# Optimization experiments

Hardware: AMD Instinct MI355X
Metric: run time of the kernel (lower is better)

The kernel has to match this reference:

```python
import jax, jax.numpy as jnp
import numpy as np

B, N, C_IN, S = 8, 50000, 32, 9
C_OUT, M, NNZ = 64, 12500, 50000


def setup_inputs() -> dict:
    key = jax.random.key(0)
    ks = jax.random.split(key, 6)
    return {
        "x": jax.random.normal(ks[0], (B, N, C_IN), dtype=jnp.float32),
        "W": jax.random.normal(ks[1], (S * C_IN, C_OUT), dtype=jnp.float32) * 0.05,
        "b": jnp.zeros((C_OUT,), dtype=jnp.float32),
        "value": jax.random.uniform(ks[2], (NNZ,), dtype=jnp.float32),
        "spiral_indices": jax.random.randint(ks[3], (N, S), 0, N),
        "row": jax.random.randint(ks[4], (NNZ,), 0, M),
        "col": jax.random.randint(ks[5], (NNZ,), 0, N),
        "dim_size": M,
    }


def reference(x, W, b, value, spiral_indices, row, col, dim_size):
    Bb, Nn, Ci = x.shape
    # SpiralConv: gather spiral neighborhoods then linear
    g = x[:, spiral_indices]                # [B, N, S, C_in]
    h = g.reshape(Bb, Nn, -1) @ W + b       # [B, N, C_out]
    h = jax.nn.elu(h)                       # ELU, alpha=1
    # Pool: sparse down-transform (index_select * value, scatter_add over rows)
    gathered = h[:, col] * value[None, :, None]            # [B, nnz, C_out]
    pooled = jax.ops.segment_sum(
        gathered.transpose(1, 0, 2), row, num_segments=dim_size
    ).transpose(1, 0, 2)                                   # [B, M, C_out]
    return pooled
```

## Files before the change

### kernel.cpp

```cpp
#include <hip/hip_runtime.h>
#include <hip/hip_bf16.h>
#include <math.h>

#define Bq    8
#define Nq    50000
#define CIN   32
#define Sq    9
#define COUT  64
#define MSEG  12500
#define NNZq  50000
#define KSTEPS 9

#define WT_BYTES  65536
#define XB_BYTES  ((size_t)Bq*Nq*CIN*2)

typedef __bf16 bf16x8 __attribute__((ext_vector_type(8)));
typedef float  f32x4  __attribute__((ext_vector_type(4)));

static __device__ __forceinline__ unsigned short f2bf(float f) {
  union { float f; unsigned u; } v; v.f = f;
  unsigned r = v.u + 0x7fffu + ((v.u >> 16) & 1u);
  return (unsigned short)(r >> 16);
}

__global__ __launch_bounds__(256) void prep_wt(const float* __restrict__ W,
                                               unsigned short* __restrict__ WT)
{
  int t = blockIdx.x * 256 + threadIdx.x;
  if (t >= 288 * 64) return;
  int c = t & 63;
  int k = t >> 6;
  int j = (c & 3) * 16 + (c >> 2);
  WT[j * 288 + k] = f2bf(W[k * 64 + c]);
}

__global__ __launch_bounds__(256) void prep_xb(const float* __restrict__ x,
                                               unsigned short* __restrict__ xb)
{
  int i = blockIdx.x * 256 + threadIdx.x;
  float4 v = ((const float4*)x)[i];
  ushort4 p;
  p.x = f2bf(v.x); p.y = f2bf(v.y); p.z = f2bf(v.z); p.w = f2bf(v.w);
  ((ushort4*)xb)[i] = p;
}

__global__ __launch_bounds__(256) void csr_hist(const int* __restrict__ row,
                                                int* __restrict__ cnt)
{
  int e = blockIdx.x * 256 + threadIdx.x;
  if (e < NNZq) atomicAdd(&cnt[row[e]], 1);
}

__global__ __launch_bounds__(1024) void csr_scan(const int* __restrict__ cnt,
                                                 int* __restrict__ start)
{
  __shared__ int s[1024];
  const int t = threadIdx.x;
  const int PER = (MSEG + 1023) / 1024;
  int loc[PER];
  int sum = 0;
  #pragma unroll
  for (int i = 0; i < PER; ++i) {
    int r = t * PER + i;
    int v = (r < MSEG) ? cnt[r] : 0;
    loc[i] = sum; sum += v;
  }
  s[t] = sum; __syncthreads();
  for (int off = 1; off < 1024; off <<= 1) {
    int v = (t >= off) ? s[t - off] : 0;
    __syncthreads();
    s[t] += v;
    __syncthreads();
  }
  int pre = (t == 0) ? 0 : s[t - 1];
  #pragma unroll
  for (int i = 0; i < PER; ++i) {
    int r = t * PER + i;
    if (r < MSEG) start[r] = pre + loc[i];
  }
}

__global__ __launch_bounds__(256) void csr_fill(const int* __restrict__ row,
                                                const int* __restrict__ start,
                                                int* __restrict__ fill,
                                                int* __restrict__ eidx)
{
  int e = blockIdx.x * 256 + threadIdx.x;
  if (e >= NNZq) return;
  int r = row[e];
  int p = start[r] + atomicAdd(&fill[r], 1);
  eidx[p] = e;
}

__global__ __launch_bounds__(256, 4) void fused_gather_gemm_elu(
    const unsigned short* __restrict__ xb, const unsigned short* __restrict__ WT,
    const float* __restrict__ bias, const int* __restrict__ sidx,
    unsigned short* __restrict__ h, int bbase, int nb, int lgnb)
{
  const int tid  = threadIdx.x;
  const int bid  = blockIdx.x;
  const int bloc = bid & (nb - 1);
  const int n0   = (bid >> lgnb) * 64;
  const int b    = bbase + bloc;

  const int w  = tid >> 6;
  const int l  = tid & 63;
  const int la = l & 15;
  const int kg = l >> 4;

  int nrow   = n0 + w * 16 + la;
  int nclamp = nrow < Nq ? nrow : Nq - 1;

  int idxs[KSTEPS];
  #pragma unroll
  for (int s = 0; s < KSTEPS; ++s) idxs[s] = sidx[nclamp * Sq + s];

  const unsigned short* xbb = xb + (size_t)b * Nq * CIN + kg * 8;
  const __bf16* wb = (const __bf16*)WT + la * 288 + kg * 8;

  bf16x8 afr[KSTEPS];
  #pragma unroll
  for (int ks = 0; ks < KSTEPS; ++ks)
    afr[ks] = *(const bf16x8*)(xbb + (size_t)idxs[ks] * CIN);

  f32x4 acc[4];
  #pragma unroll
  for (int i = 0; i < 4; ++i) acc[i] = (f32x4){0.f, 0.f, 0.f, 0.f};

  #pragma unroll
  for (int ks = 0; ks < KSTEPS; ++ks) {
    #pragma unroll
    for (int ct = 0; ct < 4; ++ct) {
      bf16x8 bb = *(const bf16x8*)(wb + ct * 16 * 288 + ks * 32);
      acc[ct] = __builtin_amdgcn_mfma_f32_16x16x32_bf16(afr[ks], bb, acc[ct], 0, 0, 0);
    }
  }

  float4 b4 = ((const float4*)bias)[la];
  #pragma unroll
  for (int r = 0; r < 4; ++r) {
    int n = n0 + w * 16 + kg * 4 + r;
    if (n < Nq) {
      float v0 = acc[0][r] + b4.x;
      float v1 = acc[1][r] + b4.y;
      float v2 = acc[2][r] + b4.z;
      float v3 = acc[3][r] + b4.w;
      v0 = v0 > 0.f ? v0 : (__expf(v0) - 1.0f);
      v1 = v1 > 0.f ? v1 : (__expf(v1) - 1.0f);
      v2 = v2 > 0.f ? v2 : (__expf(v2) - 1.0f);
      v3 = v3 > 0.f ? v3 : (__expf(v3) - 1.0f);
      ushort4 pk;
      pk.x = f2bf(v0); pk.y = f2bf(v1); pk.z = f2bf(v2); pk.w = f2bf(v3);
      *(ushort4*)&h[((size_t)n * nb + bloc) * COUT + 4 * la] = pk;
    }
  }
}

__global__ __launch_bounds__(512) void csr_pool(
    const unsigned short* __restrict__ h, const float* __restrict__ value,
    const int* __restrict__ col, const int* __restrict__ start,
    const int* __restrict__ cnt, const int* __restrict__ eidx,
    float* __restrict__ out, int bbase, int nb)
{
  int r    = blockIdx.x;
  int c    = threadIdx.x & 63;
  int bloc = threadIdx.x >> 6;
  int s0 = start[r];
  int ne = cnt[r];
  float acc = 0.f;
  int j = 0;
  for (; j + 4 <= ne; j += 4) {
    int e0 = eidx[s0+j], e1 = eidx[s0+j+1], e2 = eidx[s0+j+2], e3 = eidx[s0+j+3];
    int   c0 = col[e0],   c1 = col[e1],   c2 = col[e2],   c3 = col[e3];
    float v0 = value[e0], v1 = value[e1], v2 = value[e2], v3 = value[e3];
    unsigned short h0 = h[((size_t)c0 * nb + bloc) * COUT + c];
    unsigned short h1 = h[((size_t)c1 * nb + bloc) * COUT + c];
    unsigned short h2 = h[((size_t)c2 * nb + bloc) * COUT + c];
    unsigned short h3 = h[((size_t)c3 * nb + bloc) * COUT + c];
    acc += v0 * __bfloat162float(*(const __hip_bfloat16*)&h0)
         + v1 * __bfloat162float(*(const __hip_bfloat16*)&h1)
         + v2 * __bfloat162float(*(const __hip_bfloat16*)&h2)
         + v3 * __bfloat162float(*(const __hip_bfloat16*)&h3);
  }
  for (; j < ne; ++j) {
    int e = eidx[s0 + j];
    float v = value[e];
    int cc = col[e];
    unsigned short hv = h[((size_t)cc * nb + bloc) * COUT + c];
    acc += v * __bfloat162float(*(const __hip_bfloat16*)&hv);
  }
  out[((size_t)(bbase + bloc) * MSEG + r) * COUT + c] = acc;
}

extern "C" void kernel_launch(void* const* d_in, const int* in_sizes, int n_in,
                              void* d_out, int out_size, void* d_ws, size_t ws_size,
                              hipStream_t stream)
{
  const float* x     = (const float*)d_in[0];
  const float* W     = (const float*)d_in[1];
  const float* bias  = (const float*)d_in[2];
  const float* value = (const float*)d_in[3];
  const int*   sidx  = (const int*)d_in[4];
  const int*   row   = (const int*)d_in[5];
  const int*   col   = (const int*)d_in[6];
  float* out = (float*)d_out;

  char* p = (char*)d_ws;
  unsigned short* WT = (unsigned short*)p;          p += WT_BYTES;
  unsigned short* xb = (unsigned short*)p;          p += XB_BYTES;
  int* cnt   = (int*)p;                             p += 4 * MSEG;
  int* fill  = (int*)p;                             p += 4 * MSEG;
  int* start = (int*)p;                             p += 4 * MSEG;
  int* eidx  = (int*)p;                             p += 4 * NNZq;
  unsigned short* h = (unsigned short*)p;

  size_t fixed = (size_t)(p - (char*)d_ws);
  size_t per_batch = (size_t)Nq * COUT * 2;
  if (ws_size < fixed + per_batch) return;
  int nb_max = (int)((ws_size - fixed) / per_batch);
  int nb, lgnb;
  if      (nb_max >= 8) { nb = 8; lgnb = 3; }
  else if (nb_max >= 4) { nb = 4; lgnb = 2; }
  else if (nb_max >= 2) { nb = 2; lgnb = 1; }
  else                  { nb = 1; lgnb = 0; }

  hipMemsetAsync(cnt, 0, 8 * MSEG, stream);
  prep_wt<<<(288 * 64 + 255) / 256, 256, 0, stream>>>(W, WT);
  prep_xb<<<Bq * Nq * CIN / 4 / 256, 256, 0, stream>>>(x, xb);
  csr_hist<<<(NNZq + 255) / 256, 256, 0, stream>>>(row, cnt);
  csr_scan<<<1, 1024, 0, stream>>>(cnt, start);
  csr_fill<<<(NNZq + 255) / 256, 256, 0, stream>>>(row, start, fill, eidx);

  int nx = (Nq + 63) / 64;
  for (int bbase = 0; bbase < Bq; bbase += nb) {
    fused_gather_gemm_elu<<<nx * nb, 256, 0, stream>>>(xb, WT, bias, sidx, h,
                                                       bbase, nb, lgnb);
    csr_pool<<<MSEG, nb * 64, 0, stream>>>(h, value, col, start, cnt, eidx,
                                           out, bbase, nb);
  }
}
```

Baseline: 239.7 us.

## Pack col/value into CSR entries, batch-major h layout, add sched barrier

```diff
diff --git a/kernel.cpp b/kernel.cpp
--- a/kernel.cpp
+++ b/kernel.cpp
@@ -81,15 +81,20 @@
 }
 
 __global__ __launch_bounds__(256) void csr_fill(const int* __restrict__ row,
+                                                const int* __restrict__ col,
+                                                const float* __restrict__ value,
                                                 const int* __restrict__ start,
                                                 int* __restrict__ fill,
-                                                int* __restrict__ eidx)
+                                                int2* __restrict__ cv)
 {
   int e = blockIdx.x * 256 + threadIdx.x;
   if (e >= NNZq) return;
   int r = row[e];
   int p = start[r] + atomicAdd(&fill[r], 1);
-  eidx[p] = e;
+  int2 pk;
+  pk.x = col[e];
+  pk.y = __float_as_int(value[e]);
+  cv[p] = pk;
 }
 
 __global__ __launch_bounds__(256, 4) void fused_gather_gemm_elu(
@@ -122,6 +127,7 @@
   #pragma unroll
   for (int ks = 0; ks < KSTEPS; ++ks)
     afr[ks] = *(const bf16x8*)(xbb + (size_t)idxs[ks] * CIN);
+  __builtin_amdgcn_sched_barrier(0);
 
   f32x4 acc[4];
   #pragma unroll
@@ -151,43 +157,39 @@
       v3 = v3 > 0.f ? v3 : (__expf(v3) - 1.0f);
       ushort4 pk;
       pk.x = f2bf(v0); pk.y = f2bf(v1); pk.z = f2bf(v2); pk.w = f2bf(v3);
-      *(ushort4*)&h[((size_t)n * nb + bloc) * COUT + 4 * la] = pk;
+      *(ushort4*)&h[((size_t)bloc * Nq + n) * COUT + 4 * la] = pk;
     }
   }
 }
 
 __global__ __launch_bounds__(512) void csr_pool(
-    const unsigned short* __restrict__ h, const float* __restrict__ value,
-    const int* __restrict__ col, const int* __restrict__ start,
-    const int* __restrict__ cnt, const int* __restrict__ eidx,
+    const unsigned short* __restrict__ h, const int2* __restrict__ cv,
+    const int* __restrict__ start, const int* __restrict__ cnt,
     float* __restrict__ out, int bbase, int nb)
 {
   int r    = blockIdx.x;
   int c    = threadIdx.x & 63;
   int bloc = threadIdx.x >> 6;
+  const unsigned short* hb = h + (size_t)bloc * Nq * COUT + c;
   int s0 = start[r];
   int ne = cnt[r];
   float acc = 0.f;
   int j = 0;
   for (; j + 4 <= ne; j += 4) {
-    int e0 = eidx[s0+j], e1 = eidx[s0+j+1], e2 = eidx[s0+j+2], e3 = eidx[s0+j+3];
-    int   c0 = col[e0],   c1 = col[e1],   c2 = col[e2],   c3 = col[e3];
-    float v0 = value[e0], v1 = value[e1], v2 = value[e2], v3 = value[e3];
-    unsigned short h0 = h[((size_t)c0 * nb + bloc) * COUT + c];
-    unsigned short h1 = h[((size_t)c1 * nb + bloc) * COUT + c];
-    unsigned short h2 = h[((size_t)c2 * nb + bloc) * COUT + c];
-    unsigned short h3 = h[((size_t)c3 * nb + bloc) * COUT + c];
-    acc += v0 * __bfloat162float(*(const __hip_bfloat16*)&h0)
-         + v1 * __bfloat162float(*(const __hip_bfloat16*)&h1)
-         + v2 * __bfloat162float(*(const __hip_bfloat16*)&h2)
-         + v3 * __bfloat162float(*(const __hip_bfloat16*)&h3);
+    int2 p0 = cv[s0+j], p1 = cv[s0+j+1], p2 = cv[s0+j+2], p3 = cv[s0+j+3];
+    unsigned short h0 = hb[(size_t)p0.x * COUT];
+    unsigned short h1 = hb[(size_t)p1.x * COUT];
+    unsigned short h2 = hb[(size_t)p2.x * COUT];
+    unsigned short h3 = hb[(size_t)p3.x * COUT];
+    acc += __int_as_float(p0.y) * __bfloat162float(*(const __hip_bfloat16*)&h0)
+         + __int_as_float(p1.y) * __bfloat162float(*(const __hip_bfloat16*)&h1)
+         + __int_as_float(p2.y) * __bfloat162float(*(const __hip_bfloat16*)&h2)
+         + __int_as_float(p3.y) * __bfloat162float(*(const __hip_bfloat16*)&h3);
   }
   for (; j < ne; ++j) {
-    int e = eidx[s0 + j];
-    float v = value[e];
-    int cc = col[e];
-    unsigned short hv = h[((size_t)cc * nb + bloc) * COUT + c];
-    acc += v * __bfloat162float(*(const __hip_bfloat16*)&hv);
+    int2 pk = cv[s0 + j];
+    unsigned short hv = hb[(size_t)pk.x * COUT];
+    acc += __int_as_float(pk.y) * __bfloat162float(*(const __hip_bfloat16*)&hv);
   }
   out[((size_t)(bbase + bloc) * MSEG + r) * COUT + c] = acc;
 }
@@ -211,7 +213,7 @@
   int* cnt   = (int*)p;                             p += 4 * MSEG;
   int* fill  = (int*)p;                             p += 4 * MSEG;
   int* start = (int*)p;                             p += 4 * MSEG;
-  int* eidx  = (int*)p;                             p += 4 * NNZq;
+  int2* cv   = (int2*)p;                            p += 8 * NNZq;
   unsigned short* h = (unsigned short*)p;
 
   size_t fixed = (size_t)(p - (char*)d_ws);
@@ -229,13 +231,12 @@
   prep_xb<<<Bq * Nq * CIN / 4 / 256, 256, 0, stream>>>(x, xb);
   csr_hist<<<(NNZq + 255) / 256, 256, 0, stream>>>(row, cnt);
   csr_scan<<<1, 1024, 0, stream>>>(cnt, start);
-  csr_fill<<<(NNZq + 255) / 256, 256, 0, stream>>>(row, start, fill, eidx);
+  csr_fill<<<(NNZq + 255) / 256, 256, 0, stream>>>(row, col, value, start, fill, cv);
 
   int nx = (Nq + 63) / 64;
   for (int bbase = 0; bbase < Bq; bbase += nb) {
     fused_gather_gemm_elu<<<nx * nb, 256, 0, stream>>>(xb, WT, bias, sidx, h,
                                                        bbase, nb, lgnb);
-    csr_pool<<<MSEG, nb * 64, 0, stream>>>(h, value, col, start, cnt, eidx,
-                                           out, bbase, nb);
-  }
-}
+    csr_pool<<<MSEG, nb * 64, 0, stream>>>(h, cv, start, cnt, out, bbase, nb);
+  }
+}
```

After: 230.3 us. 3.9% less time.
